# Kernel optimization log

Hardware: AMD Instinct MI355X
Metric: run time of the kernel (lower is better)

## Reference

```python
import math
import jax, jax.numpy as jnp
import numpy as np

B, S, E = 4, 2048, 1024

def setup_inputs() -> dict:
    key = jax.random.key(0)
    k1, k2, k3 = jax.random.split(key, 3)
    X = jax.random.normal(k1, (B, S, E), dtype=jnp.float32)
    # nn.Linear(E, 3E): weight [3E, E], bias [3E]; scale weights for sane softmax
    W = jax.random.normal(k2, (3 * E, E), dtype=jnp.float32) * (1.0 / math.sqrt(E))
    b = jax.random.normal(k3, (3 * E,), dtype=jnp.float32) * 0.01
    return {"X": X, "W": W, "b": b}

def reference(X, W, b):
    E_ = X.shape[-1]
    # fused QKV projection: X @ W^T + b -> [B, S, 3E]
    qkv = jnp.einsum('bse,fe->bsf', X, W) + b
    q, k, v = jnp.split(qkv, 3, axis=-1)
    scores = jnp.einsum('bqe,bke->bqk', q, k) / math.sqrt(E_)
    attention_weight = jax.nn.softmax(scores, axis=-1)  # [B, S, S]
    output = jnp.einsum('bqk,bke->bqe', attention_weight, v)
    return (output, attention_weight)
```

## Files before the change

kernel.cpp:

```cpp
#include <hip/hip_runtime.h>
#include <math.h>

typedef __bf16 bf16;
typedef __bf16 bf16x4 __attribute__((ext_vector_type(4)));
typedef __bf16 bf16x8 __attribute__((ext_vector_type(8)));
typedef float f32x4 __attribute__((ext_vector_type(4)));

#define MODE_QKV    0
#define MODE_SCORES 1
#define MODE_PV     2

__device__ inline void gload_lds16(const bf16* g, bf16* l) {
    __builtin_amdgcn_global_load_lds(
        (const __attribute__((address_space(1))) void*)g,
        (__attribute__((address_space(3))) void*)l, 16, 0, 0);
}

#define DSR(dst, base, imm)                                                 \
    asm volatile("ds_read_b128 %0, %1 offset:%2"                            \
        : "=v"(dst)                                                         \
        : "v"((const __attribute__((address_space(3))) bf16*)(base)),       \
          "i"(imm))

#define MF(i, j) acc[i][j] = __builtin_amdgcn_mfma_f32_16x16x32_bf16(       \
    af[i], bq[j], acc[i][j], 0, 0, 0);

template <int MODE, int NT>
__global__ __launch_bounds__(512) void mfma_nt(
    const bf16* __restrict__ A, const bf16* __restrict__ B,
    const float* __restrict__ bias, void* __restrict__ Cv,
    bf16* __restrict__ Vtp,
    int lda, int ldb, int ldc,
    long sA, long sB, long sC, float alpha)
{
    A += (long)blockIdx.z * sA;
    B += (long)blockIdx.z * sB;

    __shared__ bf16 As[3 * 8192] __attribute__((aligned(16)));
    __shared__ bf16 Bs[3 * 4096] __attribute__((aligned(16)));

    const int t  = threadIdx.x;
    const int m0 = blockIdx.y * 256;
    const int n0 = blockIdx.x * 128;

    const int lane = t & 63;
    const int wave = t >> 6;
    const int wr   = (wave >> 1) * 64;
    const int wc   = (wave & 1) * 64;
    const int fr   = lane & 15;
    const int kq8  = lane >> 4;

    const bf16* gA0; const bf16* gA1; const bf16* gB0;
    {
        const int c0 = t,        r0 = c0 >> 2, h0 = ((c0 & 3) ^ ((r0 >> 1) & 3)) * 8;
        const int c1 = t + 512,  r1 = c1 >> 2, h1 = ((c1 & 3) ^ ((r1 >> 1) & 3)) * 8;
        gA0 = A + (long)(m0 + r0) * lda + h0;
        gA1 = A + (long)(m0 + r1) * lda + h1;
        gB0 = B + (long)(n0 + r0) * ldb + h0;
    }

    const int swz = kq8 ^ ((fr >> 1) & 3);
    const bf16* pA = As + (wr + fr) * 32 + swz * 8;
    const bf16* pB = Bs + (wc + fr) * 32 + swz * 8;

    f32x4 acc[4][4] = {};
    bf16x8 af[4], bq[4];
    int kofs;

#define STAGE3(SS, ko)                                                      \
    gload_lds16(gA0 + (ko), &As[(SS) * 8192 + t * 8]);                      \
    gload_lds16(gA1 + (ko), &As[(SS) * 8192 + (t + 512) * 8]);              \
    gload_lds16(gB0 + (ko), &Bs[(SS) * 4096 + t * 8]);

#define TB(CS, STG) do {                                                    \
    DSR(af[0], pA, (CS) * 16384 + 0);                                       \
    DSR(af[1], pA, (CS) * 16384 + 1024);                                    \
    DSR(bq[0], pB, (CS) * 8192 + 0);                                        \
    DSR(bq[1], pB, (CS) * 8192 + 1024);                                     \
    DSR(bq[2], pB, (CS) * 8192 + 2048);                                     \
    DSR(bq[3], pB, (CS) * 8192 + 3072);                                     \
    DSR(af[2], pA, (CS) * 16384 + 2048);                                    \
    DSR(af[3], pA, (CS) * 16384 + 3072);                                    \
    asm volatile("s_waitcnt lgkmcnt(2)" ::: "memory");                      \
    __builtin_amdgcn_sched_barrier(0);                                      \
    __builtin_amdgcn_s_setprio(1);                                          \
    MF(0,0) MF(0,1) MF(1,0) MF(1,1)                                         \
    MF(0,2) MF(0,3) MF(1,2) MF(1,3)                                         \
    __builtin_amdgcn_s_setprio(0);                                          \
    if constexpr ((STG) == 1) { STAGE3(((CS) + 2) % 3, kofs); kofs += 32; } \
    asm volatile("s_waitcnt lgkmcnt(0)" ::: "memory");                      \
    __builtin_amdgcn_sched_barrier(0);                                      \
    __builtin_amdgcn_s_setprio(1);                                          \
    MF(2,0) MF(2,1) MF(3,0) MF(3,1)                                         \
    MF(2,2) MF(2,3) MF(3,2) MF(3,3)                                         \
    __builtin_amdgcn_s_setprio(0);                                          \
    if constexpr ((STG) == 1)                                               \
        asm volatile("s_waitcnt vmcnt(3)" ::: "memory");                    \
    else if constexpr ((STG) == 0)                                          \
        asm volatile("s_waitcnt vmcnt(0)" ::: "memory");                    \
    if constexpr ((STG) != 2) __builtin_amdgcn_s_barrier();                 \
} while (0)

    STAGE3(0, 0);
    STAGE3(1, 32);
    kofs = 64;
    asm volatile("s_waitcnt vmcnt(3)" ::: "memory");
    __builtin_amdgcn_s_barrier();

    static_assert(NT % 3 != 0, "peel pattern assumes NT%3 in {1,2}");
    if constexpr (NT % 3 == 2) {
        TB(0, 1); TB(1, 1);
        for (int g = 0; g < (NT - 5) / 3; ++g) { TB(2, 1); TB(0, 1); TB(1, 1); }
        TB(2, 1); TB(0, 0); TB(1, 2);
    } else {
        TB(0, 1);
        for (int g = 0; g < (NT - 4) / 3; ++g) { TB(1, 1); TB(2, 1); TB(0, 1); }
        TB(1, 1); TB(2, 0); TB(0, 2);
    }
#undef TB
#undef STAGE3

    const int r4 = (lane >> 4) * 4;
    if constexpr (MODE == MODE_PV) {
        float* C = (float*)Cv + (long)blockIdx.z * sC;
        const float* Rs = bias + (long)blockIdx.z * 2048;
        float iv[4][4];
#pragma unroll
        for (int i = 0; i < 4; i++)
#pragma unroll
            for (int r = 0; r < 4; r++)
                iv[i][r] = Rs[m0 + wr + i * 16 + r4 + r];
#pragma unroll
        for (int j = 0; j < 4; j++) {
            const int col = n0 + wc + j * 16 + fr;
#pragma unroll
            for (int i = 0; i < 4; i++)
#pragma unroll
                for (int r = 0; r < 4; r++) {
                    const long row = m0 + wr + i * 16 + r4 + r;
                    C[row * ldc + col] = acc[i][j][r] * iv[i][r];
                }
        }
    } else if constexpr (MODE == MODE_QKV) {
        if (n0 >= 2048) {
            const int  bi = m0 >> 11;
            bf16* Vb = Vtp + (long)bi * (1024 * 2048);
#pragma unroll
            for (int j = 0; j < 4; j++) {
                const int col = n0 + wc + j * 16 + fr;
                const int e   = col - 2048;
                const float bv = bias[col];
#pragma unroll
                for (int i = 0; i < 4; i++) {
                    const int sb = (m0 + wr + i * 16 + r4) & 2047;
                    bf16x4 o = { (bf16)(acc[i][j][0] + bv),
                                 (bf16)(acc[i][j][1] + bv),
                                 (bf16)(acc[i][j][2] + bv),
                                 (bf16)(acc[i][j][3] + bv) };
                    *(bf16x4*)&Vb[(long)e * 2048 + sb] = o;
                }
            }
        } else {
            bf16* C = (bf16*)Cv;
#pragma unroll
            for (int j = 0; j < 4; j++) {
                const int col = n0 + wc + j * 16 + fr;
                const float bv = bias[col];
#pragma unroll
                for (int i = 0; i < 4; i++)
#pragma unroll
                    for (int r = 0; r < 4; r++) {
                        const long row = m0 + wr + i * 16 + r4 + r;
                        C[row * ldc + col] = (bf16)(acc[i][j][r] + bv);
                    }
            }
        }
    } else {
        bf16* C = (bf16*)Cv + (long)blockIdx.z * sC;
#pragma unroll
        for (int j = 0; j < 4; j++) {
            const int col = n0 + wc + j * 16 + fr;
#pragma unroll
            for (int i = 0; i < 4; i++)
#pragma unroll
                for (int r = 0; r < 4; r++) {
                    const long row = m0 + wr + i * 16 + r4 + r;
                    C[row * ldc + col] = (bf16)__expf(alpha * acc[i][j][r]);
                }
        }
    }
}

__global__ __launch_bounds__(256) void f32_to_bf16_2(
    const float* __restrict__ X, bf16* __restrict__ Xb, long nX,
    const float* __restrict__ W, bf16* __restrict__ Wb, long nW)
{
    long i = ((long)blockIdx.x * 256 + threadIdx.x) * 4;
    const float* in; bf16* out; long idx;
    if (i < nX) { in = X; out = Xb; idx = i; }
    else        { in = W; out = Wb; idx = i - nX; if (idx >= nW) return; }
    float4 v = *(const float4*)(in + idx);
    bf16x4 o = { (bf16)v.x, (bf16)v.y, (bf16)v.z, (bf16)v.w };
    *(bf16x4*)(out + idx) = o;
}

__global__ __launch_bounds__(256) void norm_rows(
    const bf16* __restrict__ Pu, float* __restrict__ out1,
    float* __restrict__ rs)
{
    const bf16* p = Pu  + (long)blockIdx.x * 2048;
    float* o = out1 + (long)blockIdx.x * 2048;
    const int t = threadIdx.x;
    bf16x8 v = *(const bf16x8*)(p + t * 8);
    float f[8];
    float s = 0.f;
#pragma unroll
    for (int k = 0; k < 8; k++) { f[k] = (float)v[k]; s += f[k]; }
#pragma unroll
    for (int off = 32; off > 0; off >>= 1) s += __shfl_xor(s, off);
    __shared__ float red[4];
    const int wid = t >> 6, lane = t & 63;
    if (lane == 0) red[wid] = s;
    __syncthreads();
    s = red[0] + red[1] + red[2] + red[3];
    const float inv = 1.0f / s;
    if (t == 0) rs[blockIdx.x] = inv;
    float4 a, b;
    a.x = f[0] * inv; a.y = f[1] * inv; a.z = f[2] * inv; a.w = f[3] * inv;
    b.x = f[4] * inv; b.y = f[5] * inv; b.z = f[6] * inv; b.w = f[7] * inv;
    *(float4*)(o + t * 8)     = a;
    *(float4*)(o + t * 8 + 4) = b;
}

extern "C" void kernel_launch(void* const* d_in, const int* in_sizes, int n_in,
                              void* d_out, int out_size, void* d_ws, size_t ws_size,
                              hipStream_t stream)
{
    const int B = 4, S = 2048, E = 1024;
    const float* X    = (const float*)d_in[0];
    const float* W    = (const float*)d_in[1];
    const float* bias = (const float*)d_in[2];

    float* out0 = (float*)d_out;
    float* out1 = out0 + (long)B * S * E;

    char* ws = (char*)d_ws;
    bf16*  qkvb = (bf16*)(ws);
    bf16*  Vt   = (bf16*)(ws + 33554432);
    float* rs   = (float*)(ws + 50331648);
    bf16*  Pu   = (bf16*)(ws + 67108864);
    bf16*  Xb   = (bf16*)(ws + 67108864);
    bf16*  Wb   = (bf16*)(ws + 83886080);

    const long nX = (long)B * S * E;
    const long nW = (long)3 * E * E;
    f32_to_bf16_2<<<(nX + nW) / 1024, 256, 0, stream>>>(X, Xb, nX, W, Wb, nW);

    mfma_nt<MODE_QKV, 32><<<dim3(3 * E / 128, B * S / 256, 1), 512, 0, stream>>>(
        Xb, Wb, bias, qkvb, Vt, E, E, 2048, 0, 0, 0, 1.0f);

    mfma_nt<MODE_SCORES, 32><<<dim3(S / 128, S / 256, B), 512, 0, stream>>>(
        qkvb, qkvb + 1024, nullptr, Pu, nullptr, 2048, 2048, S,
        (long)S * 2048, (long)S * 2048, (long)S * S, 0.03125f);

    norm_rows<<<B * S, 256, 0, stream>>>(Pu, out1, rs);

    mfma_nt<MODE_PV, 64><<<dim3(E / 128, S / 256, B), 512, 0, stream>>>(
        Pu, Vt, rs, out0, nullptr, S, S, E,
        (long)S * S, (long)E * S, (long)S * E, 1.0f);
}
```

Measured before the change: 288.9 us.

## Fuse softmax row-sum into scores epilogue and normalized write into PV kernel

Removes the separate norm_rows kernel. The scores kernel now reduces each row's exp sums across lanes and atomically adds them into a zeroed workspace vector. The PV kernel reads the P tiles already staged in LDS and has a subset of its blocks (chosen by k-tile index modulo the grid x) write the normalized fp32 attention weights to the output, so Pu is never re-read from global memory for normalization. This adds atomics, a memset, extra LDS reads and global stores inside the PV main loop, and slightly different summation order.

```diff
diff --git a/kernel.cpp b/kernel.cpp
--- a/kernel.cpp
+++ b/kernel.cpp
@@ -28,8 +28,8 @@
 template <int MODE, int NT>
 __global__ __launch_bounds__(512) void mfma_nt(
     const bf16* __restrict__ A, const bf16* __restrict__ B,
-    const float* __restrict__ bias, void* __restrict__ Cv,
-    bf16* __restrict__ Vtp,
+    const float* __restrict__ bias, float* __restrict__ aux,
+    void* __restrict__ Cv, bf16* __restrict__ Vtp,
     int lda, int ldb, int ldc,
     long sA, long sB, long sC, float alpha)
 {
@@ -51,21 +51,36 @@
     const int kq8  = lane >> 4;
 
     const bf16* gA0; const bf16* gA1; const bf16* gB0;
+    int h0e, h1e;
     {
-        const int c0 = t,        r0 = c0 >> 2, h0 = ((c0 & 3) ^ ((r0 >> 1) & 3)) * 8;
-        const int c1 = t + 512,  r1 = c1 >> 2, h1 = ((c1 & 3) ^ ((r1 >> 1) & 3)) * 8;
-        gA0 = A + (long)(m0 + r0) * lda + h0;
-        gA1 = A + (long)(m0 + r1) * lda + h1;
-        gB0 = B + (long)(n0 + r0) * ldb + h0;
+        const int c0 = t,        r0 = c0 >> 2;
+        const int c1 = t + 512,  r1 = c1 >> 2;
+        h0e = ((c0 & 3) ^ ((r0 >> 1) & 3)) * 8;
+        h1e = ((c1 & 3) ^ ((r1 >> 1) & 3)) * 8;
+        gA0 = A + (long)(m0 + r0) * lda + h0e;
+        gA1 = A + (long)(m0 + r1) * lda + h1e;
+        gB0 = B + (long)(n0 + r0) * ldb + h0e;
     }
 
     const int swz = kq8 ^ ((fr >> 1) & 3);
     const bf16* pA = As + (wr + fr) * 32 + swz * 8;
     const bf16* pB = Bs + (wc + fr) * 32 + swz * 8;
+    const bf16* pS0 = As + t * 8;
+    const bf16* pS1 = As + (t + 512) * 8;
 
     f32x4 acc[4][4] = {};
     bf16x8 af[4], bq[4];
+    bf16x8 ov0, ov1;
     int kofs;
+    int tcur = 0;
+    const int bxi = (int)blockIdx.x;
+
+    float iva = 0.f, ivb = 0.f;
+    if constexpr (MODE == MODE_PV) {
+        const float* Rs = bias + (long)blockIdx.z * 2048;
+        iva = 1.0f / Rs[m0 + (t >> 2)];
+        ivb = 1.0f / Rs[m0 + 128 + (t >> 2)];
+    }
 
 #define STAGE3(SS, ko)                                                      \
     gload_lds16(gA0 + (ko), &As[(SS) * 8192 + t * 8]);                      \
@@ -88,6 +103,12 @@
     MF(0,2) MF(0,3) MF(1,2) MF(1,3)                                         \
     __builtin_amdgcn_s_setprio(0);                                          \
     if constexpr ((STG) == 1) { STAGE3(((CS) + 2) % 3, kofs); kofs += 32; } \
+    if constexpr (MODE == MODE_PV) {                                        \
+        if ((tcur & 7) == bxi) {                                            \
+            DSR(ov0, pS0, (CS) * 16384);                                    \
+            DSR(ov1, pS1, (CS) * 16384);                                    \
+        }                                                                   \
+    }                                                                       \
     asm volatile("s_waitcnt lgkmcnt(0)" ::: "memory");                      \
     __builtin_amdgcn_sched_barrier(0);                                      \
     __builtin_amdgcn_s_setprio(1);                                          \
@@ -98,6 +119,27 @@
         asm volatile("s_waitcnt vmcnt(3)" ::: "memory");                    \
     else if constexpr ((STG) == 0)                                          \
         asm volatile("s_waitcnt vmcnt(0)" ::: "memory");                    \
+    if constexpr (MODE == MODE_PV) {                                        \
+        if ((tcur & 7) == bxi) {                                            \
+            float* o0 = aux + ((long)blockIdx.z * 2048 + m0 + (t >> 2))     \
+                        * 2048 + tcur * 32 + h0e;                           \
+            float* o1 = aux + ((long)blockIdx.z * 2048 + m0 + 128 + (t >> 2))\
+                        * 2048 + tcur * 32 + h1e;                           \
+            f32x4 w0 = { (float)ov0[0] * iva, (float)ov0[1] * iva,          \
+                         (float)ov0[2] * iva, (float)ov0[3] * iva };        \
+            f32x4 w1 = { (float)ov0[4] * iva, (float)ov0[5] * iva,          \
+                         (float)ov0[6] * iva, (float)ov0[7] * iva };        \
+            f32x4 w2 = { (float)ov1[0] * ivb, (float)ov1[1] * ivb,          \
+                         (float)ov1[2] * ivb, (float)ov1[3] * ivb };        \
+            f32x4 w3 = { (float)ov1[4] * ivb, (float)ov1[5] * ivb,          \
+                         (float)ov1[6] * ivb, (float)ov1[7] * ivb };        \
+            *(f32x4*)o0       = w0;                                         \
+            *(f32x4*)(o0 + 4) = w1;                                         \
+            *(f32x4*)o1       = w2;                                         \
+            *(f32x4*)(o1 + 4) = w3;                                         \
+        }                                                                   \
+        ++tcur;                                                             \
+    }                                                                       \
     if constexpr ((STG) != 2) __builtin_amdgcn_s_barrier();                 \
 } while (0)
 
@@ -129,7 +171,7 @@
         for (int i = 0; i < 4; i++)
 #pragma unroll
             for (int r = 0; r < 4; r++)
-                iv[i][r] = Rs[m0 + wr + i * 16 + r4 + r];
+                iv[i][r] = 1.0f / Rs[m0 + wr + i * 16 + r4 + r];
 #pragma unroll
         for (int j = 0; j < 4; j++) {
             const int col = n0 + wc + j * 16 + fr;
@@ -177,6 +219,7 @@
         }
     } else {
         bf16* C = (bf16*)Cv + (long)blockIdx.z * sC;
+        float rsacc[4][4] = {};
 #pragma unroll
         for (int j = 0; j < 4; j++) {
             const int col = n0 + wc + j * 16 + fr;
@@ -185,9 +228,24 @@
 #pragma unroll
                 for (int r = 0; r < 4; r++) {
                     const long row = m0 + wr + i * 16 + r4 + r;
-                    C[row * ldc + col] = (bf16)__expf(alpha * acc[i][j][r]);
+                    bf16 bv = (bf16)__expf(alpha * acc[i][j][r]);
+                    C[row * ldc + col] = bv;
+                    rsacc[i][r] += (float)bv;
                 }
         }
+#pragma unroll
+        for (int i = 0; i < 4; i++)
+#pragma unroll
+            for (int r = 0; r < 4; r++) {
+                float s = rsacc[i][r];
+                s += __shfl_xor(s, 1);
+                s += __shfl_xor(s, 2);
+                s += __shfl_xor(s, 4);
+                s += __shfl_xor(s, 8);
+                if (fr == 0)
+                    atomicAdd(&aux[(long)blockIdx.z * 2048 +
+                                   m0 + wr + i * 16 + r4 + r], s);
+            }
     }
 }
 
@@ -204,34 +262,6 @@
     *(bf16x4*)(out + idx) = o;
 }
 
-__global__ __launch_bounds__(256) void norm_rows(
-    const bf16* __restrict__ Pu, float* __restrict__ out1,
-    float* __restrict__ rs)
-{
-    const bf16* p = Pu  + (long)blockIdx.x * 2048;
-    float* o = out1 + (long)blockIdx.x * 2048;
-    const int t = threadIdx.x;
-    bf16x8 v = *(const bf16x8*)(p + t * 8);
-    float f[8];
-    float s = 0.f;
-#pragma unroll
-    for (int k = 0; k < 8; k++) { f[k] = (float)v[k]; s += f[k]; }
-#pragma unroll
-    for (int off = 32; off > 0; off >>= 1) s += __shfl_xor(s, off);
-    __shared__ float red[4];
-    const int wid = t >> 6, lane = t & 63;
-    if (lane == 0) red[wid] = s;
-    __syncthreads();
-    s = red[0] + red[1] + red[2] + red[3];
-    const float inv = 1.0f / s;
-    if (t == 0) rs[blockIdx.x] = inv;
-    float4 a, b;
-    a.x = f[0] * inv; a.y = f[1] * inv; a.z = f[2] * inv; a.w = f[3] * inv;
-    b.x = f[4] * inv; b.y = f[5] * inv; b.z = f[6] * inv; b.w = f[7] * inv;
-    *(float4*)(o + t * 8)     = a;
-    *(float4*)(o + t * 8 + 4) = b;
-}
-
 extern "C" void kernel_launch(void* const* d_in, const int* in_sizes, int n_in,
                               void* d_out, int out_size, void* d_ws, size_t ws_size,
                               hipStream_t stream)
@@ -247,7 +277,7 @@
     char* ws = (char*)d_ws;
     bf16*  qkvb = (bf16*)(ws);
     bf16*  Vt   = (bf16*)(ws + 33554432);
-    float* rs   = (float*)(ws + 50331648);
+    float* rsum = (float*)(ws + 50331648);
     bf16*  Pu   = (bf16*)(ws + 67108864);
     bf16*  Xb   = (bf16*)(ws + 67108864);
     bf16*  Wb   = (bf16*)(ws + 83886080);
@@ -256,16 +286,16 @@
     const long nW = (long)3 * E * E;
     f32_to_bf16_2<<<(nX + nW) / 1024, 256, 0, stream>>>(X, Xb, nX, W, Wb, nW);
 
+    hipMemsetAsync(rsum, 0, (size_t)B * S * sizeof(float), stream);
+
     mfma_nt<MODE_QKV, 32><<<dim3(3 * E / 128, B * S / 256, 1), 512, 0, stream>>>(
-        Xb, Wb, bias, qkvb, Vt, E, E, 2048, 0, 0, 0, 1.0f);
+        Xb, Wb, bias, nullptr, qkvb, Vt, E, E, 2048, 0, 0, 0, 1.0f);
 
     mfma_nt<MODE_SCORES, 32><<<dim3(S / 128, S / 256, B), 512, 0, stream>>>(
-        qkvb, qkvb + 1024, nullptr, Pu, nullptr, 2048, 2048, S,
+        qkvb, qkvb + 1024, nullptr, rsum, Pu, nullptr, 2048, 2048, S,
         (long)S * 2048, (long)S * 2048, (long)S * S, 0.03125f);
 
-    norm_rows<<<B * S, 256, 0, stream>>>(Pu, out1, rs);
-
     mfma_nt<MODE_PV, 64><<<dim3(E / 128, S / 256, B), 512, 0, stream>>>(
-        Pu, Vt, rs, out0, nullptr, S, S, E,
+        Pu, Vt, rsum, out1, out0, nullptr, S, S, E,
         (long)S * S, (long)E * S, (long)S * E, 1.0f);
 }
```

Result: slower. 297.9 us (+3.1%).
